# Optimization experiments

Measured on AMD Instinct MI355X. Metric: run time of the kernel, lower is better.

The kernel has to match this reference:

```python
import jax, jax.numpy as jnp
import numpy as np

N_NODES = 50000
N_EDGES = 800000
IN_FEAT = 128
N_CLASSES = 64
K_HOPS = 2


def setup_inputs() -> dict:
    key = jax.random.key(0)
    k1, k2, k3, k4 = jax.random.split(key, 4)
    x = jax.random.normal(k1, (N_NODES, IN_FEAT), dtype=jnp.float32)
    edge_index = jax.random.randint(k2, (2, N_EDGES), 0, N_NODES, dtype=jnp.int64)
    # Linear layer params (PyTorch-style Kaiming-uniform-ish scale)
    lim = 1.0 / np.sqrt(IN_FEAT)
    W = jax.random.uniform(k3, (N_CLASSES, IN_FEAT), jnp.float32, -lim, lim)
    b = jax.random.uniform(k4, (N_CLASSES,), jnp.float32, -lim, lim)
    return {"x": x, "edge_index": edge_index, "W": W, "b": b}


def _sg_propagate(x, edge_index, K):
    """K-hop GCN-normalized propagation with self-loops (SGConv)."""
    N = x.shape[0]
    loop = jnp.arange(N, dtype=edge_index.dtype)
    row = jnp.concatenate([edge_index[0], loop])  # source nodes
    col = jnp.concatenate([edge_index[1], loop])  # target nodes
    deg = jax.ops.segment_sum(jnp.ones_like(col, dtype=x.dtype), col, num_segments=N)
    dinv = jnp.where(deg > 0, jax.lax.rsqrt(deg), 0.0)
    norm = dinv[row] * dinv[col]  # [E+N]
    for _ in range(K):
        x = jax.ops.segment_sum(norm[:, None] * x[row], col, num_segments=N)
    return x


def reference(x, edge_index, W, b):
    h = _sg_propagate(x, edge_index, K_HOPS)  # [N, in_features]
    return h @ W.T + b  # [N, num_classes]
```

## Files before the change

### kernel.cpp

```cpp
#include <hip/hip_runtime.h>
#include <hip/hip_fp16.h>

#define N_NODES   50000
#define N_EDGES   800000
#define IN_FEAT   128
#define N_CLASSES 64
#define LDS_PAD   132

__global__ void zero_cnt_kernel(int* __restrict__ cnt, int n) {
    int i = blockIdx.x * blockDim.x + threadIdx.x;
    if (i < n) cnt[i] = 0;
}

__global__ void count_rank_kernel(const int* __restrict__ col, int* __restrict__ cnt,
                                  int* __restrict__ rank, int e) {
    int i = blockIdx.x * blockDim.x + threadIdx.x;
    if (i < e) rank[i] = atomicAdd(&cnt[col[i]], 1);
}

__global__ __launch_bounds__(256) void block_sum_kernel(const int* __restrict__ cnt,
                                                        int* __restrict__ bsum, int n) {
    __shared__ int s[256];
    int t = threadIdx.x;
    int i = blockIdx.x * 256 + t;
    s[t] = (i < n) ? cnt[i] : 0;
    __syncthreads();
    for (int off = 128; off > 0; off >>= 1) {
        if (t < off) s[t] += s[t + off];
        __syncthreads();
    }
    if (t == 0) bsum[blockIdx.x] = s[0];
}

__global__ __launch_bounds__(256) void scan_bsum_kernel(int* __restrict__ bsum, int nb) {
    __shared__ int s[256];
    int t = threadIdx.x;
    s[t] = (t < nb) ? bsum[t] : 0;
    __syncthreads();
    for (int off = 1; off < 256; off <<= 1) {
        int add = (t >= off) ? s[t - off] : 0;
        __syncthreads();
        s[t] += add;
        __syncthreads();
    }
    if (t < nb) bsum[t] = s[t];
}

__global__ __launch_bounds__(256) void apply_scan_kernel(const int* __restrict__ cnt,
                                                         const int* __restrict__ bsum,
                                                         int* __restrict__ rowptr,
                                                         float* __restrict__ dinv, int n) {
    __shared__ int s[256];
    int b = blockIdx.x, t = threadIdx.x;
    int i = b * 256 + t;
    int v = (i < n) ? cnt[i] : 0;
    s[t] = v;
    __syncthreads();
    for (int off = 1; off < 256; off <<= 1) {
        int add = (t >= off) ? s[t - off] : 0;
        __syncthreads();
        s[t] += add;
        __syncthreads();
    }
    int boff = (b > 0) ? bsum[b - 1] : 0;
    if (i < n) {
        rowptr[i] = boff + s[t] - v;
        dinv[i]   = rsqrtf((float)(v + 1));
    }
    if (i == n - 1) rowptr[n] = boff + s[t];
}

__global__ void scatter_kernel(const int* __restrict__ row, const int* __restrict__ col,
                               const int* __restrict__ rank, const int* __restrict__ rowptr,
                               int* __restrict__ adj, int e) {
    int i = blockIdx.x * blockDim.x + threadIdx.x;
    if (i < e) adj[rowptr[col[i]] + rank[i]] = row[i];
}

__global__ __launch_bounds__(256) void gemm_kernel(const float* __restrict__ x,
                                                   const float* __restrict__ W,
                                                   const float* __restrict__ dinv,
                                                   __half* __restrict__ u, int n) {
    __shared__ float xs[64][LDS_PAD];
    __shared__ float ws[64][LDS_PAD];
    int t = threadIdx.x;
    int rowbase = blockIdx.x * 64;

    for (int i = t; i < 64 * 32; i += 256) {
        int r  = i >> 5;
        int kk = i & 31;
        *(float4*)(&ws[r][kk * 4]) = *(const float4*)(W + (size_t)r * IN_FEAT + kk * 4);
        int gr = rowbase + r;
        float4 v = make_float4(0.f, 0.f, 0.f, 0.f);
        if (gr < n) v = *(const float4*)(x + (size_t)gr * IN_FEAT + kk * 4);
        *(float4*)(&xs[r][kk * 4]) = v;
    }
    __syncthreads();

    int rg = t >> 4;
    int cg = t & 15;
    float acc[4][4] = {};

    for (int kk = 0; kk < 32; ++kk) {
        float4 a[4], bb[4];
#pragma unroll
        for (int i = 0; i < 4; ++i) a[i]  = *(float4*)(&xs[rg + 16 * i][kk * 4]);
#pragma unroll
        for (int j = 0; j < 4; ++j) bb[j] = *(float4*)(&ws[cg + 16 * j][kk * 4]);
#pragma unroll
        for (int i = 0; i < 4; ++i)
#pragma unroll
            for (int j = 0; j < 4; ++j)
                acc[i][j] += a[i].x * bb[j].x + a[i].y * bb[j].y +
                             a[i].z * bb[j].z + a[i].w * bb[j].w;
    }

#pragma unroll
    for (int i = 0; i < 4; ++i) {
        int gr = rowbase + rg + 16 * i;
        if (gr < n) {
            float d = dinv[gr];
#pragma unroll
            for (int j = 0; j < 4; ++j)
                u[(size_t)gr * N_CLASSES + cg + 16 * j] = __float2half(d * acc[i][j]);
        }
    }
}

__global__ __launch_bounds__(256) void hop_sum_kernel(const int* __restrict__ rowptr,
                                                      const int* __restrict__ adj,
                                                      const float* __restrict__ dinv,
                                                      const __half* __restrict__ yin,
                                                      __half* __restrict__ yout_h,
                                                      float* __restrict__ yout_f,
                                                      const float* __restrict__ bias,
                                                      int mode, int n) {
    int sub  = threadIdx.x >> 6;
    int lane = threadIdx.x & 63;
    int node = blockIdx.x * 4 + sub;
    if (node >= n) return;

    int s  = rowptr[node];
    int e2 = rowptr[node + 1];

    float acc = __half2float(yin[(size_t)node * N_CLASSES + lane]);
    int k = s;
    for (; k + 7 < e2; k += 8) {
        float v0 = __half2float(yin[(size_t)adj[k + 0] * N_CLASSES + lane]);
        float v1 = __half2float(yin[(size_t)adj[k + 1] * N_CLASSES + lane]);
        float v2 = __half2float(yin[(size_t)adj[k + 2] * N_CLASSES + lane]);
        float v3 = __half2float(yin[(size_t)adj[k + 3] * N_CLASSES + lane]);
        float v4 = __half2float(yin[(size_t)adj[k + 4] * N_CLASSES + lane]);
        float v5 = __half2float(yin[(size_t)adj[k + 5] * N_CLASSES + lane]);
        float v6 = __half2float(yin[(size_t)adj[k + 6] * N_CLASSES + lane]);
        float v7 = __half2float(yin[(size_t)adj[k + 7] * N_CLASSES + lane]);
        acc += ((v0 + v1) + (v2 + v3)) + ((v4 + v5) + (v6 + v7));
    }
    for (; k < e2; ++k)
        acc += __half2float(yin[(size_t)adj[k] * N_CLASSES + lane]);

    float d = dinv[node];
    if (mode == 0) {
        yout_h[(size_t)node * N_CLASSES + lane] = __float2half(d * d * acc);
    } else {
        yout_f[(size_t)node * N_CLASSES + lane] = d * acc + bias[lane];
    }
}

extern "C" void kernel_launch(void* const* d_in, const int* in_sizes, int n_in,
                              void* d_out, int out_size, void* d_ws, size_t ws_size,
                              hipStream_t stream) {
    const float* x     = (const float*)d_in[0];
    const int*   edges = (const int*)d_in[1];
    const float* W     = (const float*)d_in[2];
    const float* b     = (const float*)d_in[3];
    float*       out   = (float*)d_out;

    const int* row = edges;
    const int* col = edges + N_EDGES;

    char* ws = (char*)d_ws;
    int*     cnt    = (int*)(ws + 0);
    int*     rowptr = (int*)(ws + 256 * 1024);
    float*   dinv   = (float*)(ws + 512 * 1024);
    int*     bsum   = (int*)(ws + 768 * 1024);
    int*     adj    = (int*)(ws + 1024 * 1024);
    int*     rank   = (int*)(ws + 4608 * 1024);
    __half*  u      = (__half*)(ws + 8 * 1024 * 1024);
    __half*  w1     = (__half*)(ws + 16 * 1024 * 1024);

    const int nblk = (N_NODES + 255) / 256;

    zero_cnt_kernel<<<nblk, 256, 0, stream>>>(cnt, N_NODES);
    count_rank_kernel<<<(N_EDGES + 255) / 256, 256, 0, stream>>>(col, cnt, rank, N_EDGES);
    block_sum_kernel<<<nblk, 256, 0, stream>>>(cnt, bsum, N_NODES);
    scan_bsum_kernel<<<1, 256, 0, stream>>>(bsum, nblk);
    apply_scan_kernel<<<nblk, 256, 0, stream>>>(cnt, bsum, rowptr, dinv, N_NODES);
    scatter_kernel<<<(N_EDGES + 255) / 256, 256, 0, stream>>>(row, col, rank, rowptr, adj, N_EDGES);

    gemm_kernel<<<(N_NODES + 63) / 64, 256, 0, stream>>>(x, W, dinv, u, N_NODES);

    hop_sum_kernel<<<(N_NODES + 3) / 4, 256, 0, stream>>>(rowptr, adj, dinv,
        u, w1, nullptr, nullptr, 0, N_NODES);
    hop_sum_kernel<<<(N_NODES + 3) / 4, 256, 0, stream>>>(rowptr, adj, dinv,
        w1, nullptr, out, b, 1, N_NODES);
}
```

Measured before the change: 159.1 us.

## Use 16-bit adjacency, vectorize edge kernels, fold block-sum scan into apply

Stores CSR neighbor indices as unsigned short instead of int, halving adjacency bytes read in both hop passes. The count and scatter kernels now handle four edges per thread with int4 loads. The separate single-block scan of block sums is removed, and every apply_scan block rescans the block sums itself, saving one launch at the cost of redundant work. The 16-bit indices rely on the node count (50000) fitting below 65536, which holds for this fixed size but is not general.

```diff
diff --git a/kernel.cpp b/kernel.cpp
--- a/kernel.cpp
+++ b/kernel.cpp
@@ -14,8 +14,17 @@
 
 __global__ void count_rank_kernel(const int* __restrict__ col, int* __restrict__ cnt,
                                   int* __restrict__ rank, int e) {
-    int i = blockIdx.x * blockDim.x + threadIdx.x;
-    if (i < e) rank[i] = atomicAdd(&cnt[col[i]], 1);
+    int i = (blockIdx.x * blockDim.x + threadIdx.x) * 4;
+    if (i + 3 < e) {
+        int4 c = *(const int4*)(col + i);
+        int r0 = atomicAdd(&cnt[c.x], 1);
+        int r1 = atomicAdd(&cnt[c.y], 1);
+        int r2 = atomicAdd(&cnt[c.z], 1);
+        int r3 = atomicAdd(&cnt[c.w], 1);
+        *(int4*)(rank + i) = make_int4(r0, r1, r2, r3);
+    } else {
+        for (int k = i; k < e; ++k) rank[k] = atomicAdd(&cnt[col[k]], 1);
+    }
 }
 
 __global__ __launch_bounds__(256) void block_sum_kernel(const int* __restrict__ cnt,
@@ -32,26 +41,24 @@
     if (t == 0) bsum[blockIdx.x] = s[0];
 }
 
-__global__ __launch_bounds__(256) void scan_bsum_kernel(int* __restrict__ bsum, int nb) {
-    __shared__ int s[256];
-    int t = threadIdx.x;
-    s[t] = (t < nb) ? bsum[t] : 0;
-    __syncthreads();
-    for (int off = 1; off < 256; off <<= 1) {
-        int add = (t >= off) ? s[t - off] : 0;
-        __syncthreads();
-        s[t] += add;
-        __syncthreads();
-    }
-    if (t < nb) bsum[t] = s[t];
-}
-
 __global__ __launch_bounds__(256) void apply_scan_kernel(const int* __restrict__ cnt,
                                                          const int* __restrict__ bsum,
                                                          int* __restrict__ rowptr,
-                                                         float* __restrict__ dinv, int n) {
+                                                         float* __restrict__ dinv,
+                                                         int n, int nch) {
+    __shared__ int sb[256];
     __shared__ int s[256];
     int b = blockIdx.x, t = threadIdx.x;
+
+    sb[t] = (t < nch) ? bsum[t] : 0;
+    __syncthreads();
+    for (int off = 1; off < 256; off <<= 1) {
+        int add = (t >= off) ? sb[t - off] : 0;
+        __syncthreads();
+        sb[t] += add;
+        __syncthreads();
+    }
+
     int i = b * 256 + t;
     int v = (i < n) ? cnt[i] : 0;
     s[t] = v;
@@ -62,7 +69,7 @@
         s[t] += add;
         __syncthreads();
     }
-    int boff = (b > 0) ? bsum[b - 1] : 0;
+    int boff = (b > 0) ? sb[b - 1] : 0;
     if (i < n) {
         rowptr[i] = boff + s[t] - v;
         dinv[i]   = rsqrtf((float)(v + 1));
@@ -72,9 +79,20 @@
 
 __global__ void scatter_kernel(const int* __restrict__ row, const int* __restrict__ col,
                                const int* __restrict__ rank, const int* __restrict__ rowptr,
-                               int* __restrict__ adj, int e) {
-    int i = blockIdx.x * blockDim.x + threadIdx.x;
-    if (i < e) adj[rowptr[col[i]] + rank[i]] = row[i];
+                               unsigned short* __restrict__ adj, int e) {
+    int i = (blockIdx.x * blockDim.x + threadIdx.x) * 4;
+    if (i + 3 < e) {
+        int4 r  = *(const int4*)(row + i);
+        int4 c  = *(const int4*)(col + i);
+        int4 rk = *(const int4*)(rank + i);
+        adj[rowptr[c.x] + rk.x] = (unsigned short)r.x;
+        adj[rowptr[c.y] + rk.y] = (unsigned short)r.y;
+        adj[rowptr[c.z] + rk.z] = (unsigned short)r.z;
+        adj[rowptr[c.w] + rk.w] = (unsigned short)r.w;
+    } else {
+        for (int k = i; k < e; ++k)
+            adj[rowptr[col[k]] + rank[k]] = (unsigned short)row[k];
+    }
 }
 
 __global__ __launch_bounds__(256) void gemm_kernel(const float* __restrict__ x,
@@ -128,7 +146,7 @@
 }
 
 __global__ __launch_bounds__(256) void hop_sum_kernel(const int* __restrict__ rowptr,
-                                                      const int* __restrict__ adj,
+                                                      const unsigned short* __restrict__ adj,
                                                       const float* __restrict__ dinv,
                                                       const __half* __restrict__ yin,
                                                       __half* __restrict__ yout_h,
@@ -180,23 +198,23 @@
     const int* col = edges + N_EDGES;
 
     char* ws = (char*)d_ws;
-    int*     cnt    = (int*)(ws + 0);
-    int*     rowptr = (int*)(ws + 256 * 1024);
-    float*   dinv   = (float*)(ws + 512 * 1024);
-    int*     bsum   = (int*)(ws + 768 * 1024);
-    int*     adj    = (int*)(ws + 1024 * 1024);
-    int*     rank   = (int*)(ws + 4608 * 1024);
-    __half*  u      = (__half*)(ws + 8 * 1024 * 1024);
-    __half*  w1     = (__half*)(ws + 16 * 1024 * 1024);
-
-    const int nblk = (N_NODES + 255) / 256;
+    int*            cnt    = (int*)(ws + 0);
+    int*            rowptr = (int*)(ws + 256 * 1024);
+    float*          dinv   = (float*)(ws + 512 * 1024);
+    int*            bsum   = (int*)(ws + 768 * 1024);
+    unsigned short* adj    = (unsigned short*)(ws + 1024 * 1024);
+    int*            rank   = (int*)(ws + 4608 * 1024);
+    __half*         u      = (__half*)(ws + 8 * 1024 * 1024);
+    __half*         w1     = (__half*)(ws + 16 * 1024 * 1024);
+
+    const int nblk  = (N_NODES + 255) / 256;
+    const int eblk4 = (N_EDGES / 4 + 255) / 256;
 
     zero_cnt_kernel<<<nblk, 256, 0, stream>>>(cnt, N_NODES);
-    count_rank_kernel<<<(N_EDGES + 255) / 256, 256, 0, stream>>>(col, cnt, rank, N_EDGES);
+    count_rank_kernel<<<eblk4, 256, 0, stream>>>(col, cnt, rank, N_EDGES);
     block_sum_kernel<<<nblk, 256, 0, stream>>>(cnt, bsum, N_NODES);
-    scan_bsum_kernel<<<1, 256, 0, stream>>>(bsum, nblk);
-    apply_scan_kernel<<<nblk, 256, 0, stream>>>(cnt, bsum, rowptr, dinv, N_NODES);
-    scatter_kernel<<<(N_EDGES + 255) / 256, 256, 0, stream>>>(row, col, rank, rowptr, adj, N_EDGES);
+    apply_scan_kernel<<<nblk, 256, 0, stream>>>(cnt, bsum, rowptr, dinv, N_NODES, nblk);
+    scatter_kernel<<<eblk4, 256, 0, stream>>>(row, col, rank, rowptr, adj, N_EDGES);
 
     gemm_kernel<<<(N_NODES + 63) / 64, 256, 0, stream>>>(x, W, dinv, u, N_NODES);
 
```

Measured after the change: 156.8 us. Within noise of the previous version (-1.5%).
